# Optimization experiments

Measured on AMD Instinct MI355X. Metric: run time of the kernel, lower is better.

The kernel has to match this reference:

```python
import jax, jax.numpy as jnp
import numpy as np

B, LQ, LK, D, H = 4, 2048, 2048, 1024, 16
HD = D // H  # head dim = 64


def setup_inputs() -> dict:
    key = jax.random.key(0)
    ks = jax.random.split(key, 8)
    s = 1.0 / np.sqrt(D)
    return {
        "zt": jax.random.normal(ks[0], (B, LQ, D), jnp.float32),
        "ic": jax.random.normal(ks[1], (B, LK, D), jnp.float32),
        "Wq": jax.random.normal(ks[2], (D, D), jnp.float32) * s,
        "bq": jax.random.normal(ks[3], (D,), jnp.float32) * 0.01,
        "Wk": jax.random.normal(ks[4], (D, D), jnp.float32) * s,
        "bk": jax.random.normal(ks[5], (D,), jnp.float32) * 0.01,
        "Wv": jax.random.normal(ks[6], (D, D), jnp.float32) * s,
        "bv": jax.random.normal(ks[7], (D,), jnp.float32) * 0.01,
    }


def reference(zt, ic, Wq, bq, Wk, bk, Wv, bv):
    # Linear projections (torch Linear: x @ W.T + b); weights here stored as [out, in]
    q = zt @ Wq.T + bq            # [B, LQ, D]
    k = ic @ Wk.T + bk            # [B, LK, D]
    v = ic @ Wv.T + bv            # [B, LK, D]
    # split heads -> [B, H, L, HD]
    q = q.reshape(B, LQ, H, HD).transpose(0, 2, 1, 3)
    k = k.reshape(B, LK, H, HD).transpose(0, 2, 1, 3)
    v = v.reshape(B, LK, H, HD).transpose(0, 2, 1, 3)
    scale = 1.0 / jnp.sqrt(jnp.asarray(HD, q.dtype))
    scores = jnp.einsum('bhqd,bhkd->bhqk', q, k) * scale  # [B, H, LQ, LK]
    attn = jax.nn.softmax(scores, axis=-1)
    out = jnp.einsum('bhqk,bhkd->bhqd', attn, v)          # [B, H, LQ, HD]
    return out.transpose(0, 2, 1, 3).reshape(B, LQ, D)
```

## Files before the change

### kernel.cpp

```cpp
#include <hip/hip_runtime.h>
#include <hip/hip_bf16.h>
#include <cstdint>

#define B_  4
#define LQ_ 2048
#define LK_ 2048
#define D_  1024
#define H_  16
#define HD_ 64

typedef __attribute__((ext_vector_type(8))) short bf16x8;
typedef __attribute__((ext_vector_type(4))) float f32x4;

#if defined(__has_builtin)
#if __has_builtin(__builtin_amdgcn_exp2f)
#define EXP2F(x) __builtin_amdgcn_exp2f(x)
#else
#define EXP2F(x) exp2f(x)
#endif
#else
#define EXP2F(x) exp2f(x)
#endif

__device__ __forceinline__ unsigned short f2b(float f) {
    union { float f; unsigned u; } v; v.f = f;
    unsigned u = v.u;
    unsigned r = (u + 0x7fffu + ((u >> 16) & 1u)) >> 16;
    return (unsigned short)r;
}

__device__ __forceinline__ void gl_lds16(const unsigned short* g, unsigned short* l) {
    __builtin_amdgcn_global_load_lds(
        (const __attribute__((address_space(1))) unsigned int*)(g),
        (__attribute__((address_space(3))) unsigned int*)(l),
        16, 0, 0);
}

__global__ void cvt_all(const float* __restrict__ a0, unsigned short* __restrict__ d0,
                        const float* __restrict__ a1, unsigned short* __restrict__ d1,
                        const float* __restrict__ w0, unsigned short* __restrict__ e0, float s0,
                        const float* __restrict__ w1, unsigned short* __restrict__ e1,
                        const float* __restrict__ w2, unsigned short* __restrict__ e2,
                        int nact, int nw) {
    const float* in; unsigned short* out; float s = 1.0f; int n;
    switch (blockIdx.y) {
        case 0: in = a0; out = d0; n = nact; break;
        case 1: in = a1; out = d1; n = nact; break;
        case 2: in = w0; out = e0; n = nw; s = s0; break;
        case 3: in = w1; out = e1; n = nw; break;
        default: in = w2; out = e2; n = nw; break;
    }
    int i = (blockIdx.x * blockDim.x + threadIdx.x) * 8;
    int stride = gridDim.x * blockDim.x * 8;
    for (; i < n; i += stride) {
        float4 x = *(const float4*)(in + i);
        float4 y = *(const float4*)(in + i + 4);
        bf16x8 v;
        v[0] = (short)f2b(x.x * s); v[1] = (short)f2b(x.y * s);
        v[2] = (short)f2b(x.z * s); v[3] = (short)f2b(x.w * s);
        v[4] = (short)f2b(y.x * s); v[5] = (short)f2b(y.y * s);
        v[6] = (short)f2b(y.z * s); v[7] = (short)f2b(y.w * s);
        *(bf16x8*)(out + i) = v;
    }
}

__global__ __launch_bounds__(256) void qkv_gemm(
    const unsigned short* __restrict__ Xq,
    const unsigned short* __restrict__ Xkv,
    const unsigned short* __restrict__ Wqb, const unsigned short* __restrict__ Wkb,
    const unsigned short* __restrict__ Wvb,
    const float* __restrict__ bq, const float* __restrict__ bk,
    const float* __restrict__ bv, float qscale,
    unsigned short* __restrict__ Qb, unsigned short* __restrict__ Kb,
    unsigned short* __restrict__ Vb)
{
    __shared__ unsigned short As[16 * 512];
    __shared__ unsigned short Bs[16 * 512];

    const int proj = blockIdx.x >> 3;
    const int nt0  = blockIdx.x & 7;
    const unsigned short* X = (proj == 0) ? Xq : Xkv;
    const unsigned short* W = (proj == 0) ? Wqb : (proj == 1 ? Wkb : Wvb);
    const float* bias       = (proj == 0) ? bq  : (proj == 1 ? bk  : bv);
    unsigned short* Y       = (proj == 0) ? Qb  : (proj == 1 ? Kb  : Vb);
    const float bscale      = (proj == 0) ? qscale : 1.0f;

    const int tid  = threadIdx.x;
    const int lane = tid & 63;
    const int w    = tid >> 6;
    const int wm   = w & 1, wn = w >> 1;
    const int m0   = blockIdx.y * 128;
    const int n0   = nt0 * 128;
    const int l15  = lane & 15, quad = lane >> 4;

    f32x4 acc[4][4] = {};

    const unsigned short* gA[4];
    const unsigned short* gB[4];
    unsigned short* lA[4];
    unsigned short* lB[4];
    #pragma unroll
    for (int j = 0; j < 4; ++j) {
        int rt = w + (j >> 1) * 4, kblk = j & 1;
        int f = rt * 2 + kblk;
        gA[j] = X + (size_t)(m0 + rt * 16 + l15) * 1024 + kblk * 32 + quad * 8;
        gB[j] = W + (size_t)(n0 + rt * 16 + l15) * 1024 + kblk * 32 + quad * 8;
        lA[j] = &As[f * 512 + lane * 8];
        lB[j] = &Bs[f * 512 + lane * 8];
    }
    const unsigned short* frA = &As[(wm * 4) * 1024 + lane * 8];
    const unsigned short* frB = &Bs[(wn * 4) * 1024 + lane * 8];

    for (int k0 = 0; k0 < 1024; k0 += 64) {
        __syncthreads();
        #pragma unroll
        for (int j = 0; j < 4; ++j) {
            gl_lds16(gA[j] + k0, lA[j]);
            gl_lds16(gB[j] + k0, lB[j]);
        }
        __syncthreads();

        #pragma unroll
        for (int kblk = 0; kblk < 2; ++kblk) {
            bf16x8 af[4], bf[4];
            #pragma unroll
            for (int mt = 0; mt < 4; ++mt)
                af[mt] = *(const bf16x8*)(frA + mt * 1024 + kblk * 512);
            #pragma unroll
            for (int nt = 0; nt < 4; ++nt)
                bf[nt] = *(const bf16x8*)(frB + nt * 1024 + kblk * 512);
            #pragma unroll
            for (int mt = 0; mt < 4; ++mt)
                #pragma unroll
                for (int nt = 0; nt < 4; ++nt)
                    acc[mt][nt] = __builtin_amdgcn_mfma_f32_16x16x32_bf16(
                        af[mt], bf[nt], acc[mt][nt], 0, 0, 0);
        }
    }

    float bvv[4];
    #pragma unroll
    for (int nt = 0; nt < 4; ++nt)
        bvv[nt] = bias[n0 + wn * 64 + nt * 16 + l15] * bscale;

    #pragma unroll
    for (int mt = 0; mt < 4; ++mt) {
        #pragma unroll
        for (int r = 0; r < 4; ++r) {
            int row = m0 + wm * 64 + mt * 16 + quad * 4 + r;
            unsigned short* yp = Y + (size_t)row * 1024 + n0 + wn * 64;
            #pragma unroll
            for (int nt = 0; nt < 4; ++nt)
                yp[nt * 16 + l15] = f2b(acc[mt][nt][r] + bvv[nt]);
        }
    }
}

__global__ __launch_bounds__(256) void transpose_v(
    const unsigned short* __restrict__ Vb, unsigned short* __restrict__ Vt)
{
    __shared__ unsigned short L[64 * 72];
    const int t0 = blockIdx.x * 64, h = blockIdx.y, b = blockIdx.z;
    const int rr = threadIdx.x >> 3;
    const int cc = (threadIdx.x & 7) * 8;

    #pragma unroll
    for (int p = 0; p < 2; ++p) {
        int r = rr + p * 32;
        *(bf16x8*)(&L[r * 72 + cc]) =
            *(const bf16x8*)(Vb + (size_t)(b * 2048 + t0 + r) * 1024 + h * 64 + cc);
    }
    __syncthreads();
    #pragma unroll
    for (int p = 0; p < 2; ++p) {
        int d = rr + p * 32;
        bf16x8 v;
        #pragma unroll
        for (int j = 0; j < 8; ++j)
            v[j] = (short)L[(cc + j) * 72 + d];
        *(bf16x8*)(Vt + ((size_t)(b * 16 + h) * 64 + d) * 2048 + t0 + cc) = v;
    }
}

__global__ __launch_bounds__(256, 2) void attn_kernel(
    const unsigned short* __restrict__ Q,
    const unsigned short* __restrict__ Kp,
    const unsigned short* __restrict__ Vt,
    float* __restrict__ Out)
{
    __shared__ unsigned short Ks[16 * 512];
    __shared__ unsigned short Vs[16 * 512];
    __shared__ unsigned short Ps[4][4096];

    const int tid  = threadIdx.x;
    const int lane = tid & 63;
    const int w    = tid >> 6;
    const int l15  = lane & 15, quad = lane >> 4;
    const int b = blockIdx.z, h = blockIdx.y, qt = blockIdx.x;

    bf16x8 qf[4][2];
    #pragma unroll
    for (int half = 0; half < 4; ++half) {
        const unsigned short* qptr =
            Q + (size_t)(b * LQ_ + qt * 256 + w * 64 + half * 16 + l15) * 1024 + h * 64;
        qf[half][0] = *(const bf16x8*)(qptr + quad * 8);
        qf[half][1] = *(const bf16x8*)(qptr + 32 + quad * 8);
    }

    bf16x8 ones;
    #pragma unroll
    for (int j = 0; j < 8; ++j) ones[j] = (short)0x3F80;

    f32x4 oacc[4][4] = {};
    f32x4 lacc[4]    = {};

    const unsigned short* Kbase = Kp + (size_t)b * LK_ * 1024 + h * 64;
    const unsigned short* Vbase = Vt + (size_t)(b * 16 + h) * 64 * 2048;

    const unsigned short* gK[4];
    unsigned short* lK[4];
    const unsigned short* gV[4];
    unsigned short* lV[4];
    #pragma unroll
    for (int j = 0; j < 4; ++j) {
        int kt = w + (j >> 1) * 4, dblk = j & 1;
        gK[j] = Kbase + (size_t)(kt * 16 + l15) * 1024 + dblk * 32 + quad * 8;
        lK[j] = &Ks[(kt * 2 + dblk) * 512 + lane * 8];
        gV[j] = Vbase + (size_t)(w * 16 + l15) * 2048 + j * 32 + quad * 8;
        lV[j] = &Vs[(w * 4 + j) * 512 + lane * 8];
    }

    const int pws = (quad >> 1) * 128 + l15 * 8 + (quad & 1) * 4;
    unsigned short* PwB = &Ps[w][pws];
    const unsigned short* PrB = &Ps[w][lane * 8];
    const unsigned short* Kfr = &Ks[lane * 8];
    const unsigned short* Vfr = &Vs[lane * 8];

    for (int k0 = 0; k0 < LK_; k0 += 128) {
        __syncthreads();
        #pragma unroll
        for (int j = 0; j < 4; ++j) {
            gl_lds16(gK[j] + (size_t)k0 * 1024, lK[j]);
            gl_lds16(gV[j] + k0, lV[j]);
        }
        __syncthreads();

        #pragma unroll
        for (int cc = 0; cc < 2; ++cc) {
            f32x4 st[4][4] = {};
            #pragma unroll
            for (int t = 0; t < 4; ++t)
                #pragma unroll
                for (int dblk = 0; dblk < 2; ++dblk) {
                    bf16x8 kf = *(const bf16x8*)(Kfr + ((cc * 4 + t) * 2 + dblk) * 512);
                    #pragma unroll
                    for (int half = 0; half < 4; ++half)
                        st[half][t] = __builtin_amdgcn_mfma_f32_16x16x32_bf16(
                            kf, qf[half][dblk], st[half][t], 0, 0, 0);
                }

            #pragma unroll
            for (int half = 0; half < 4; ++half) {
                unsigned short* pw = PwB + half * 1024;
                #pragma unroll
                for (int t = 0; t < 4; ++t) {
                    unsigned u0 = __float_as_uint(EXP2F(st[half][t][0])) + 0x8000u;
                    unsigned u1 = __float_as_uint(EXP2F(st[half][t][1])) + 0x8000u;
                    unsigned u2 = __float_as_uint(EXP2F(st[half][t][2])) + 0x8000u;
                    unsigned u3 = __float_as_uint(EXP2F(st[half][t][3])) + 0x8000u;
                    uint2 pk;
                    pk.x = __builtin_amdgcn_perm(u1, u0, 0x07060302);
                    pk.y = __builtin_amdgcn_perm(u3, u2, 0x07060302);
                    *(uint2*)(pw + t * 256) = pk;
                }
            }

            #pragma unroll
            for (int hbl = 0; hbl < 2; ++hbl) {
                bf16x8 pf[4];
                #pragma unroll
                for (int half = 0; half < 4; ++half) {
                    pf[half] = *(const bf16x8*)(PrB + half * 1024 + hbl * 512);
                    lacc[half] = __builtin_amdgcn_mfma_f32_16x16x32_bf16(
                        pf[half], ones, lacc[half], 0, 0, 0);
                }
                int hb = cc * 2 + hbl;
                #pragma unroll
                for (int nt = 0; nt < 4; ++nt) {
                    bf16x8 vf = *(const bf16x8*)(Vfr + (nt * 4 + hb) * 512);
                    #pragma unroll
                    for (int half = 0; half < 4; ++half)
                        oacc[half][nt] = __builtin_amdgcn_mfma_f32_16x16x32_bf16(
                            pf[half], vf, oacc[half][nt], 0, 0, 0);
                }
            }
        }
    }

    #pragma unroll
    for (int half = 0; half < 4; ++half) {
        float il[4];
        #pragma unroll
        for (int r = 0; r < 4; ++r) il[r] = 1.0f / lacc[half][r];
        #pragma unroll
        for (int nt = 0; nt < 4; ++nt) {
            #pragma unroll
            for (int r = 0; r < 4; ++r) {
                size_t orow = (size_t)(b * LQ_ + qt * 256 + w * 64 + half * 16 + quad * 4 + r);
                Out[orow * 1024 + h * 64 + nt * 16 + l15] = oacc[half][nt][r] * il[r];
            }
        }
    }
}

extern "C" void kernel_launch(void* const* d_in, const int* in_sizes, int n_in,
                              void* d_out, int out_size, void* d_ws, size_t ws_size,
                              hipStream_t stream) {
    const float* zt = (const float*)d_in[0];
    const float* ic = (const float*)d_in[1];
    const float* Wq = (const float*)d_in[2];
    const float* bq = (const float*)d_in[3];
    const float* Wk = (const float*)d_in[4];
    const float* bk = (const float*)d_in[5];
    const float* Wv = (const float*)d_in[6];
    const float* bv = (const float*)d_in[7];
    float* out = (float*)d_out;

    const size_t M8 = (size_t)8192 * 1024;
    const size_t M1 = (size_t)1024 * 1024;
    unsigned short* Qb  = (unsigned short*)d_ws;
    unsigned short* Kb  = Qb  + M8;
    unsigned short* Vb  = Kb  + M8;
    unsigned short* Xz  = Vb  + M8;
    unsigned short* Xi  = Xz  + M8;
    unsigned short* Wqb = Xi  + M8;
    unsigned short* Wkb = Wqb + M1;
    unsigned short* Wvb = Wkb + M1;
    unsigned short* Vtb = Xz;

    const float qscale = 0.125f * 1.44269504088896f;

    dim3 gcv(4096, 5);
    cvt_all<<<gcv, 256, 0, stream>>>(zt, Xz, ic, Xi,
                                     Wq, Wqb, qscale, Wk, Wkb, Wv, Wvb,
                                     (int)M8, (int)M1);

    dim3 gproj(24, 64);
    qkv_gemm<<<gproj, 256, 0, stream>>>(Xz, Xi, Wqb, Wkb, Wvb,
                                        bq, bk, bv, qscale, Qb, Kb, Vb);

    dim3 gtr(32, 16, 4);
    transpose_v<<<gtr, 256, 0, stream>>>(Vb, Vtb);

    dim3 gattn(8, 16, 4);
    attn_kernel<<<gattn, 256, 0, stream>>>(Qb, Kb, Vtb, out);
}
```

Before: 318.1 us.

## Double-buffer LDS tiles in QKV projection GEMM to overlap loads with MFMA

```diff
diff --git a/kernel.cpp b/kernel.cpp
--- a/kernel.cpp
+++ b/kernel.cpp
@@ -74,8 +74,10 @@
     unsigned short* __restrict__ Qb, unsigned short* __restrict__ Kb,
     unsigned short* __restrict__ Vb)
 {
-    __shared__ unsigned short As[16 * 512];
-    __shared__ unsigned short Bs[16 * 512];
+    __shared__ unsigned short As0[16 * 512];
+    __shared__ unsigned short Bs0[16 * 512];
+    __shared__ unsigned short As1[16 * 512];
+    __shared__ unsigned short Bs1[16 * 512];
 
     const int proj = blockIdx.x >> 3;
     const int nt0  = blockIdx.x & 7;
@@ -97,38 +99,42 @@
 
     const unsigned short* gA[4];
     const unsigned short* gB[4];
-    unsigned short* lA[4];
-    unsigned short* lB[4];
+    int lofs[4];
     #pragma unroll
     for (int j = 0; j < 4; ++j) {
         int rt = w + (j >> 1) * 4, kblk = j & 1;
         int f = rt * 2 + kblk;
         gA[j] = X + (size_t)(m0 + rt * 16 + l15) * 1024 + kblk * 32 + quad * 8;
         gB[j] = W + (size_t)(n0 + rt * 16 + l15) * 1024 + kblk * 32 + quad * 8;
-        lA[j] = &As[f * 512 + lane * 8];
-        lB[j] = &Bs[f * 512 + lane * 8];
-    }
-    const unsigned short* frA = &As[(wm * 4) * 1024 + lane * 8];
-    const unsigned short* frB = &Bs[(wn * 4) * 1024 + lane * 8];
-
-    for (int k0 = 0; k0 < 1024; k0 += 64) {
-        __syncthreads();
+        lofs[j] = f * 512 + lane * 8;
+    }
+    const int frAo = (wm * 4) * 1024 + lane * 8;
+    const int frBo = (wn * 4) * 1024 + lane * 8;
+
+    #pragma unroll
+    for (int j = 0; j < 4; ++j) {
+        gl_lds16(gA[j], &As0[lofs[j]]);
+        gl_lds16(gB[j], &Bs0[lofs[j]]);
+    }
+    __syncthreads();
+
+    #pragma unroll 1
+    for (int i = 0; i < 8; ++i) {
+        const int k0 = i * 128;
         #pragma unroll
         for (int j = 0; j < 4; ++j) {
-            gl_lds16(gA[j] + k0, lA[j]);
-            gl_lds16(gB[j] + k0, lB[j]);
-        }
-        __syncthreads();
-
+            gl_lds16(gA[j] + k0 + 64, &As1[lofs[j]]);
+            gl_lds16(gB[j] + k0 + 64, &Bs1[lofs[j]]);
+        }
         #pragma unroll
         for (int kblk = 0; kblk < 2; ++kblk) {
             bf16x8 af[4], bf[4];
             #pragma unroll
             for (int mt = 0; mt < 4; ++mt)
-                af[mt] = *(const bf16x8*)(frA + mt * 1024 + kblk * 512);
+                af[mt] = *(const bf16x8*)(&As0[frAo + mt * 1024 + kblk * 512]);
             #pragma unroll
             for (int nt = 0; nt < 4; ++nt)
-                bf[nt] = *(const bf16x8*)(frB + nt * 1024 + kblk * 512);
+                bf[nt] = *(const bf16x8*)(&Bs0[frBo + nt * 1024 + kblk * 512]);
             #pragma unroll
             for (int mt = 0; mt < 4; ++mt)
                 #pragma unroll
@@ -136,6 +142,32 @@
                     acc[mt][nt] = __builtin_amdgcn_mfma_f32_16x16x32_bf16(
                         af[mt], bf[nt], acc[mt][nt], 0, 0, 0);
         }
+        __syncthreads();
+
+        if (i < 7) {
+            #pragma unroll
+            for (int j = 0; j < 4; ++j) {
+                gl_lds16(gA[j] + k0 + 128, &As0[lofs[j]]);
+                gl_lds16(gB[j] + k0 + 128, &Bs0[lofs[j]]);
+            }
+        }
+        #pragma unroll
+        for (int kblk = 0; kblk < 2; ++kblk) {
+            bf16x8 af[4], bf[4];
+            #pragma unroll
+            for (int mt = 0; mt < 4; ++mt)
+                af[mt] = *(const bf16x8*)(&As1[frAo + mt * 1024 + kblk * 512]);
+            #pragma unroll
+            for (int nt = 0; nt < 4; ++nt)
+                bf[nt] = *(const bf16x8*)(&Bs1[frBo + nt * 1024 + kblk * 512]);
+            #pragma unroll
+            for (int mt = 0; mt < 4; ++mt)
+                #pragma unroll
+                for (int nt = 0; nt < 4; ++nt)
+                    acc[mt][nt] = __builtin_amdgcn_mfma_f32_16x16x32_bf16(
+                        af[mt], bf[nt], acc[mt][nt], 0, 0, 0);
+        }
+        __syncthreads();
     }
 
     float bvv[4];
```

After: 321.5 us. About the same (+1.1%).
